# Performance work log

Measured on AMD Instinct MI355X. Metric: run time of the kernel, lower is better.

Reference implementation:

```python
import jax, jax.numpy as jnp
import numpy as np
from jax import lax

EPS = 1e-5  # BatchNorm1d default eps

def setup_inputs() -> dict:
    key = jax.random.key(0)
    ks = jax.random.split(key, 8)
    B, IN, H, T = 1024, 128, 256, 256
    return {
        "inputs": jax.random.normal(ks[0], (B, IN), jnp.float32),
        "hidden": jnp.zeros((B, H), jnp.float32),
        "W_ih": jax.random.normal(ks[1], (3 * H, IN), jnp.float32) * 0.05,
        "b_ih": jax.random.normal(ks[2], (3 * H,), jnp.float32) * 0.05,
        "W_hh": jax.random.normal(ks[3], (3 * H, H), jnp.float32) * 0.05,
        "b_hh": jax.random.normal(ks[4], (3 * H,), jnp.float32) * 0.05,
        "W_lin": jax.random.normal(ks[5], (IN, H), jnp.float32) * 0.05,
        "b_lin": jax.random.normal(ks[6], (IN,), jnp.float32) * 0.05,
        "n_frames": 256,
    }

def reference(inputs, hidden, W_ih, b_ih, W_hh, b_hh, W_lin, b_lin, n_frames):
    def step(carry, _):
        x, h = carry
        gi = x @ W_ih.T + b_ih          # [B, 3H]
        gh = h @ W_hh.T + b_hh          # [B, 3H]
        i_r, i_z, i_n = jnp.split(gi, 3, axis=-1)
        h_r, h_z, h_n = jnp.split(gh, 3, axis=-1)
        r = jax.nn.sigmoid(i_r + h_r)
        z = jax.nn.sigmoid(i_z + h_z)
        n = jnp.tanh(i_n + r * h_n)
        h_new = (1.0 - z) * n + z * h   # GRUCell update
        y = h_new @ W_lin.T + b_lin     # fed back as next input
        return (y, h_new), y

    _, ys = lax.scan(step, (inputs, hidden), None, length=n_frames)  # [T, B, out]
    # BatchNorm1d(affine=False), training mode: biased batch stats per timestep
    mean = jnp.mean(ys, axis=1, keepdims=True)
    var = jnp.var(ys, axis=1, keepdims=True)
    return (ys - mean) / jnp.sqrt(var + EPS)
```

## Files before the change

kernel.cpp:

```cpp
#include <hip/hip_runtime.h>


typedef _Float16 half8 __attribute__((ext_vector_type(8)));
typedef float floatx4 __attribute__((ext_vector_type(4)));
typedef unsigned uintx4 __attribute__((ext_vector_type(4)));

#define EPS_BN 1e-5f

#define WS_WC 0
#define WS_W0 524288
#define WS_WL 1114112
#define WS_B0 1179648
#define WS_BC 1183744
#define WS_ST 1187840

static __device__ __forceinline__ unsigned short f2h(float f) {
    union { _Float16 h; unsigned short u; } v;
    v.h = (_Float16)f;
    return v.u;
}
static __device__ __forceinline__ half8 as_h8(uint4 v) {
    union { uint4 u; half8 h; } x; x.u = v; return x.h;
}
static __device__ __forceinline__ half8 ld_agpr(const uint4* p) {
    uintx4 v = *(const uintx4*)p;
    asm volatile("; wpin" : "+a"(v));
    union { uintx4 u; half8 h; } x; x.u = v; return x.h;
}
static __device__ __forceinline__ float sigm(float x) {
    return __builtin_amdgcn_rcpf(1.0f + __builtin_amdgcn_exp2f(-1.442695041f * x));
}
static __device__ __forceinline__ float tanh_fast(float x) {
    return 1.0f - 2.0f * __builtin_amdgcn_rcpf(1.0f + __builtin_amdgcn_exp2f(2.885390082f * x));
}
static __device__ __forceinline__ void bar_lgkm() {
    asm volatile("s_waitcnt lgkmcnt(0)\n\ts_barrier" ::: "memory");
}
#define MFMA16(A, B, C) __builtin_amdgcn_mfma_f32_16x16x32_f16((A), (B), (C), 0, 0, 0)

__global__ void pack_w0_kernel(const float* __restrict__ W_ih, const float* __restrict__ W_hh,
                               const float* __restrict__ W_lin, const float* __restrict__ b_ih,
                               const float* __restrict__ b_hh,
                               uint4* __restrict__ w0, uint4* __restrict__ wl,
                               float4* __restrict__ bias0)
{
    int i = blockIdx.x * 256 + threadIdx.x;
    if (i < 36864) {
        int lane = i & 63, tile = i >> 6;
        int w = tile / 36, rem = tile - w * 36;
        int g = rem / 12, kt = rem - g * 12;
        int n = g * 256 + (w << 4) + (lane & 15);
        int k0 = (kt << 5) + ((lane >> 4) << 3);
        const float* p = (k0 < 128) ? (W_ih + n * 128 + k0)
                                    : (W_hh + n * 256 + (k0 - 128));
        unsigned short h[8];
        #pragma unroll
        for (int j = 0; j < 8; ++j) h[j] = f2h(p[j]);
        uint4 v;
        v.x = (unsigned)h[0] | ((unsigned)h[1] << 16);
        v.y = (unsigned)h[2] | ((unsigned)h[3] << 16);
        v.z = (unsigned)h[4] | ((unsigned)h[5] << 16);
        v.w = (unsigned)h[6] | ((unsigned)h[7] << 16);
        w0[i] = v;
    } else if (i < 40960) {
        int i2 = i - 36864;
        int lane = i2 & 63, tile = i2 >> 6;
        int n = (tile >> 3) * 16 + (lane & 15);
        int k0 = ((tile & 7) << 5) + ((lane >> 4) << 3);
        const float* p = W_lin + n * 256 + k0;
        unsigned short h[8];
        #pragma unroll
        for (int j = 0; j < 8; ++j) h[j] = f2h(p[j]);
        uint4 v;
        v.x = (unsigned)h[0] | ((unsigned)h[1] << 16);
        v.y = (unsigned)h[2] | ((unsigned)h[3] << 16);
        v.z = (unsigned)h[4] | ((unsigned)h[5] << 16);
        v.w = (unsigned)h[6] | ((unsigned)h[7] << 16);
        wl[i2] = v;
    } else if (i < 41216) {
        int cb = i - 40960;
        bias0[cb] = make_float4(b_ih[cb] + b_hh[cb],
                                b_ih[256 + cb] + b_hh[256 + cb],
                                b_ih[512 + cb], b_hh[512 + cb]);
    }
}

__global__ void pack_wc_kernel(const float* __restrict__ W_ih, const float* __restrict__ W_hh,
                               const float* __restrict__ W_lin, const float* __restrict__ b_ih,
                               const float* __restrict__ b_hh, const float* __restrict__ b_lin,
                               uint4* __restrict__ wc, float4* __restrict__ bc)
{
    int i = blockIdx.x * 256 + threadIdx.x;
    if (i < 32768) {
        int lane = i & 63, tile = i >> 6;
        int w = tile >> 5, r = tile & 31;
        int g = r >> 3, kt = r & 7;
        int c = (w << 4) + (lane & 15);
        int k0 = (kt << 5) + ((lane >> 4) << 3);
        float s[8];
        if (g == 3) {
            #pragma unroll
            for (int j = 0; j < 8; ++j) s[j] = W_hh[(512 + c) * 256 + k0 + j];
        } else {
            int row = g * 256 + c;
            const float* wi = W_ih + row * 128;
            #pragma unroll
            for (int j = 0; j < 8; ++j) s[j] = 0.0f;
            for (int ii = 0; ii < 128; ++ii) {
                float wv = wi[ii];
                const float* wrow = W_lin + ii * 256 + k0;
                #pragma unroll
                for (int j = 0; j < 8; ++j) s[j] += wv * wrow[j];
            }
            if (g < 2) {
                #pragma unroll
                for (int j = 0; j < 8; ++j) s[j] += W_hh[row * 256 + k0 + j];
            }
        }
        unsigned short h[8];
        #pragma unroll
        for (int j = 0; j < 8; ++j) h[j] = f2h(s[j]);
        uint4 v;
        v.x = (unsigned)h[0] | ((unsigned)h[1] << 16);
        v.y = (unsigned)h[2] | ((unsigned)h[3] << 16);
        v.z = (unsigned)h[4] | ((unsigned)h[5] << 16);
        v.w = (unsigned)h[6] | ((unsigned)h[7] << 16);
        wc[i] = v;
    } else if (i < 33024) {
        int c = i - 32768;
        float d0 = 0.f, d1 = 0.f, d2 = 0.f;
        for (int ii = 0; ii < 128; ++ii) {
            float bl = b_lin[ii];
            d0 += bl * W_ih[c * 128 + ii];
            d1 += bl * W_ih[(256 + c) * 128 + ii];
            d2 += bl * W_ih[(512 + c) * 128 + ii];
        }
        bc[c] = make_float4(b_ih[c] + b_hh[c] + d0,
                            b_ih[256 + c] + b_hh[256 + c] + d1,
                            b_ih[512 + c] + d2,
                            b_hh[512 + c]);
    }
}

__global__ __launch_bounds__(512, 2) void gru_kernel(
    const float* __restrict__ inputs,
    const float* __restrict__ hidden,
    const uint4* __restrict__ wc,
    const uint4* __restrict__ w0,
    const float4* __restrict__ bias0,
    const float4* __restrict__ bcp,
    float* __restrict__ out)
{
    __shared__ uint4 lds[9472];

    const int tid  = threadIdx.x;
    const int lane = tid & 63;
    const int w    = tid >> 6;
    const int quad = lane >> 4;
    const int nc   = lane & 15;
    const int r0   = blockIdx.x << 4;
    const int c0   = (w << 4) + nc;
    const int c1   = 128 + c0;
    const float4 bc0 = bcp[c0];
    const float4 bc1 = bcp[c1];
    const uint4* wcw0 = wc + (size_t)w * 2048;
    const uint4* wcw1 = wc + (size_t)(w + 8) * 2048;

    half8 wr0[8], wz0[8], wr1[8], wz1[8];
    #pragma unroll
    for (int kt = 0; kt < 8; ++kt) {
        wr0[kt] = ld_agpr(&wcw0[kt * 64 + lane]);
        wz0[kt] = ld_agpr(&wcw0[(8 + kt) * 64 + lane]);
        wr1[kt] = ld_agpr(&wcw1[kt * 64 + lane]);
        wz1[kt] = ld_agpr(&wcw1[(8 + kt) * 64 + lane]);
    }

    const int wbase = 1280 + (w << 10);
    #pragma unroll
    for (int i = 0; i < 4; ++i) {
        lds[wbase + (i << 6) + lane]             = wcw0[(16 + i) * 64 + lane];
        lds[wbase + ((4 + i) << 6) + lane]       = wcw0[(24 + i) * 64 + lane];
        lds[wbase + 512 + (i << 6) + lane]       = wcw1[(16 + i) * 64 + lane];
        lds[wbase + 512 + ((4 + i) << 6) + lane] = wcw1[(24 + i) * 64 + lane];
    }

    float hreg[8];
    #pragma unroll
    for (int d = 0; d < 4; ++d) {
        hreg[d]     = hidden[(r0 + (quad << 2) + d) * 256 + c0];
        hreg[4 + d] = hidden[(r0 + (quad << 2) + d) * 256 + c1];
    }

    unsigned short* lds_u16 = (unsigned short*)lds;
    const int kp  = ((w & 1) << 4) + nc;
    const int lf  = ((kp >> 3) << 4) + (quad << 2);
    const int hfb0 = (((w >> 1) * 64 + lf) << 3) + (kp & 7);
    const int hfb1 = (((4 + (w >> 1)) * 64 + lf) << 3) + (kp & 7);

    for (int idx = tid; idx < 2048; idx += 512) {
        int ktl = idx >> 8;
        int rem = idx & 255;
        int lfr = rem >> 2, jg = rem & 3;
        int m = lfr & 15;
        int hc = ktl * 32 + (lfr >> 4) * 8 + jg * 2;
        const float* p = hidden + (r0 + m) * 256 + hc;
        unsigned pk = (unsigned)f2h(p[0]) | ((unsigned)f2h(p[1]) << 16);
        ((unsigned*)lds)[(ktl * 64 + lfr) * 4 + jg] = pk;
    }
    for (int idx = tid; idx < 1024; idx += 512) {
        int kt = idx >> 8, lfr = (idx >> 2) & 63, jg = idx & 3;
        int m = lfr & 15;
        int k0 = (kt << 5) + ((lfr >> 4) << 3) + (jg << 1);
        const float* p = inputs + (r0 + m) * 128 + k0;
        unsigned pk = (unsigned)f2h(p[0]) | ((unsigned)f2h(p[1]) << 16);
        ((unsigned*)lds)[(1024 + (kt << 6) + lfr) * 4 + jg] = pk;
    }
    __syncthreads();

    unsigned short* Hout = (unsigned short*)out;

    {
        #pragma unroll
        for (int g2 = 0; g2 < 2; ++g2) {
            const uint4* ww = w0 + (size_t)(g2 ? (w + 8) : w) * 2304;
            floatx4 ar = {0.f,0.f,0.f,0.f}, az = {0.f,0.f,0.f,0.f};
            floatx4 ain = {0.f,0.f,0.f,0.f}, ahn = {0.f,0.f,0.f,0.f};
            #pragma unroll
            for (int kt = 0; kt < 12; ++kt) {
                half8 A = as_h8(kt < 4 ? lds[1024 + (kt << 6) + lane]
                                       : lds[((kt - 4) << 6) + lane]);
                ar = MFMA16(A, as_h8(ww[kt * 64 + lane]), ar);
                az = MFMA16(A, as_h8(ww[(12 + kt) * 64 + lane]), az);
                if (kt < 4)
                    ain = MFMA16(A, as_h8(ww[(24 + kt) * 64 + lane]), ain);
                else
                    ahn = MFMA16(A, as_h8(ww[(24 + kt) * 64 + lane]), ahn);
            }
            const int cc = g2 ? c1 : c0;
            const int hfb = g2 ? hfb1 : hfb0;
            float4 b0 = bias0[cc];
            #pragma unroll
            for (int d = 0; d < 4; ++d) {
                float rr = sigm(ar[d] + b0.x);
                float zz = sigm(az[d] + b0.y);
                float nn = tanh_fast(ain[d] + b0.z + rr * (ahn[d] + b0.w));
                float hnew = (1.0f - zz) * nn + zz * hreg[(g2 << 2) + d];
                hreg[(g2 << 2) + d] = hnew;
                unsigned short hu = f2h(hnew);
                lds_u16[4096 + hfb + (d << 3)] = hu;
                Hout[((size_t)(r0 + (quad << 2) + d) << 8) + cc] = hu;
            }
        }
        bar_lgkm();
    }

    for (int t = 1; t < 256; ++t) {
        const int rb   = (t & 1) << 9;
        const int wb16 = (((t + 1) & 1) << 9) << 3;

        const uint4* s0p = wcw0 + lane;
        const uint4* s1p = wcw1 + lane;
        asm("" : "+v"(s0p), "+v"(s1p));

        uint4 si0[4], sh0[4], si1[4], sh1[4];
        si0[0] = s0p[20 * 64]; sh0[0] = s0p[28 * 64];
        si1[0] = s1p[20 * 64]; sh1[0] = s1p[28 * 64];

        floatx4 ar0 = {0.f,0.f,0.f,0.f}, az0 = {0.f,0.f,0.f,0.f};
        floatx4 ai0 = {0.f,0.f,0.f,0.f}, ah0 = {0.f,0.f,0.f,0.f};
        floatx4 ar1 = {0.f,0.f,0.f,0.f}, az1 = {0.f,0.f,0.f,0.f};
        floatx4 ai1 = {0.f,0.f,0.f,0.f}, ah1 = {0.f,0.f,0.f,0.f};

        #pragma unroll
        for (int kt = 0; kt < 8; ++kt) {
            half8 A = as_h8(lds[rb + (kt << 6) + lane]);
            if (kt == 1) {
                si0[1] = s0p[21 * 64]; sh0[1] = s0p[29 * 64];
                si1[1] = s1p[21 * 64]; sh1[1] = s1p[29 * 64];
            }
            if (kt == 2) {
                si0[2] = s0p[22 * 64]; sh0[2] = s0p[30 * 64];
                si1[2] = s1p[22 * 64]; sh1[2] = s1p[30 * 64];
            }
            if (kt == 3) {
                si0[3] = s0p[23 * 64]; sh0[3] = s0p[31 * 64];
                si1[3] = s1p[23 * 64]; sh1[3] = s1p[31 * 64];
            }
            ar0 = MFMA16(A, wr0[kt], ar0);
            ar1 = MFMA16(A, wr1[kt], ar1);
            az0 = MFMA16(A, wz0[kt], az0);
            az1 = MFMA16(A, wz1[kt], az1);
            half8 Bi0 = (kt < 4) ? as_h8(lds[wbase + (kt << 6) + lane])
                                 : as_h8(si0[kt - 4]);
            half8 Bi1 = (kt < 4) ? as_h8(lds[wbase + 512 + (kt << 6) + lane])
                                 : as_h8(si1[kt - 4]);
            ai0 = MFMA16(A, Bi0, ai0);
            ai1 = MFMA16(A, Bi1, ai1);
            half8 Bh0 = (kt < 4) ? as_h8(lds[wbase + ((4 + kt) << 6) + lane])
                                 : as_h8(sh0[kt - 4]);
            half8 Bh1 = (kt < 4) ? as_h8(lds[wbase + 512 + ((4 + kt) << 6) + lane])
                                 : as_h8(sh1[kt - 4]);
            ah0 = MFMA16(A, Bh0, ah0);
            ah1 = MFMA16(A, Bh1, ah1);
        }

        const size_t obase = (size_t)t * 1024 + r0 + (quad << 2);
        #pragma unroll
        for (int d = 0; d < 4; ++d) {
            float rr = sigm(ar0[d] + bc0.x);
            float zz = sigm(az0[d] + bc0.y);
            float nn = tanh_fast(ai0[d] + bc0.z + rr * (ah0[d] + bc0.w));
            float hnew = (1.0f - zz) * nn + zz * hreg[d];
            hreg[d] = hnew;
            unsigned short hu = f2h(hnew);
            lds_u16[wb16 + hfb0 + (d << 3)] = hu;
            Hout[((obase + d) << 8) + c0] = hu;
        }
        #pragma unroll
        for (int d = 0; d < 4; ++d) {
            float rr = sigm(ar1[d] + bc1.x);
            float zz = sigm(az1[d] + bc1.y);
            float nn = tanh_fast(ai1[d] + bc1.z + rr * (ah1[d] + bc1.w));
            float hnew = (1.0f - zz) * nn + zz * hreg[4 + d];
            hreg[4 + d] = hnew;
            unsigned short hu = f2h(hnew);
            lds_u16[wb16 + hfb1 + (d << 3)] = hu;
            Hout[((obase + d) << 8) + c1] = hu;
        }
        bar_lgkm();
    }
}

__global__ __launch_bounds__(256) void ygemm_kernel(
    const uint4* __restrict__ wl, const float* __restrict__ b_lin,
    float* __restrict__ out, float* __restrict__ stats)
{
    __shared__ unsigned short sh[16 * 264];
    const int tid = threadIdx.x;
    const int t = blockIdx.x >> 6;
    const int r0 = (blockIdx.x & 63) << 4;

    {
        int row = tid >> 4, seg = tid & 15;
        const uint4* src = (const uint4*)((const unsigned short*)out
                         + (((size_t)t << 10) + r0 + row) * 256) + (seg << 1);
        uint4 a = src[0], b = src[1];
        uint4* dst = (uint4*)(sh + row * 264 + (seg << 4));
        dst[0] = a; dst[1] = b;
    }
    __syncthreads();

    const int lane = tid & 63, w = tid >> 6;
    const int quad = lane >> 4, nc = lane & 15;
    const int m = lane & 15, khi = lane >> 4;

    half8 B0[8], B1[8];
    #pragma unroll
    for (int kt = 0; kt < 8; ++kt) {
        B0[kt] = as_h8(wl[(((w << 1) + 0) * 8 + kt) * 64 + lane]);
        B1[kt] = as_h8(wl[(((w << 1) + 1) * 8 + kt) * 64 + lane]);
    }
    floatx4 a0 = {0.f,0.f,0.f,0.f}, a1 = {0.f,0.f,0.f,0.f};
    #pragma unroll
    for (int kt = 0; kt < 8; ++kt) {
        half8 A = *(const half8*)(sh + m * 264 + (kt << 5) + (khi << 3));
        a0 = MFMA16(A, B0[kt], a0);
        a1 = MFMA16(A, B1[kt], a1);
    }
    #pragma unroll
    for (int g = 0; g < 2; ++g) {
        floatx4 acc = g ? a1 : a0;
        int i = (((w << 1) + g) << 4) + nc;
        float bl = b_lin[i];
        float s1 = 0.f, s2 = 0.f;
        float* orow = out + (((size_t)t << 10) + r0 + (quad << 2)) * 128 + i;
        #pragma unroll
        for (int d = 0; d < 4; ++d) {
            float y = acc[d] + bl;
            orow[(size_t)d << 7] = y;
            s1 += y; s2 += y * y;
        }
        s1 += __shfl_xor(s1, 16); s1 += __shfl_xor(s1, 32);
        s2 += __shfl_xor(s2, 16); s2 += __shfl_xor(s2, 32);
        if (lane < 16) {
            int si = ((t << 7) + (((w << 1) + g) << 4) + lane) << 1;
            atomicAdd(&stats[si], s1);
            atomicAdd(&stats[si + 1], s2);
        }
    }
}

__global__ void norm_kernel(float* __restrict__ out, const float* __restrict__ stats)
{
    __shared__ float smean[128], sscale[128];
    int t = blockIdx.x >> 2, q = blockIdx.x & 3;
    int tid = threadIdx.x;
    if (tid < 128) {
        int si = ((t << 7) + tid) << 1;
        float mean = stats[si] * (1.0f / 1024.0f);
        float var = stats[si + 1] * (1.0f / 1024.0f) - mean * mean;
        smean[tid] = mean;
        sscale[tid] = rsqrtf(var + EPS_BN);
    }
    __syncthreads();
    float4* p = (float4*)(out + ((size_t)t << 17) + ((size_t)q << 15));
    for (int i = tid; i < 8192; i += 256) {
        int cc = (i & 31) << 2;
        float4 v = p[i];
        v.x = (v.x - smean[cc])     * sscale[cc];
        v.y = (v.y - smean[cc + 1]) * sscale[cc + 1];
        v.z = (v.z - smean[cc + 2]) * sscale[cc + 2];
        v.w = (v.w - smean[cc + 3]) * sscale[cc + 3];
        p[i] = v;
    }
}

extern "C" void kernel_launch(void* const* d_in, const int* in_sizes, int n_in,
                              void* d_out, int out_size, void* d_ws, size_t ws_size,
                              hipStream_t stream) {
    (void)in_sizes; (void)n_in; (void)out_size; (void)ws_size;
    const float* inputs = (const float*)d_in[0];
    const float* hidden = (const float*)d_in[1];
    const float* W_ih   = (const float*)d_in[2];
    const float* b_ih   = (const float*)d_in[3];
    const float* W_hh   = (const float*)d_in[4];
    const float* b_hh   = (const float*)d_in[5];
    const float* W_lin  = (const float*)d_in[6];
    const float* b_lin  = (const float*)d_in[7];

    char* ws = (char*)d_ws;
    uint4*  wcp   = (uint4*)(ws + WS_WC);
    uint4*  w0p   = (uint4*)(ws + WS_W0);
    uint4*  wlp   = (uint4*)(ws + WS_WL);
    float4* bias0 = (float4*)(ws + WS_B0);
    float4* bcp   = (float4*)(ws + WS_BC);
    float*  stats = (float*)(ws + WS_ST);

    hipMemsetAsync(stats, 0, 262144, stream);
    pack_w0_kernel<<<161, 256, 0, stream>>>(W_ih, W_hh, W_lin, b_ih, b_hh, w0p, wlp, bias0);
    pack_wc_kernel<<<129, 256, 0, stream>>>(W_ih, W_hh, W_lin, b_ih, b_hh, b_lin, wcp, bcp);
    gru_kernel<<<64, 512, 0, stream>>>(inputs, hidden, wcp, w0p, bias0, bcp, (float*)d_out);
    ygemm_kernel<<<16384, 256, 0, stream>>>(wlp, b_lin, (float*)d_out, stats);
    norm_kernel<<<1024, 256, 0, stream>>>((float*)d_out, stats);
}
```

Before: 1.047 ms.

## Fuse output GEMM with BatchNorm per timestep and merge packing kernels

The separate y-GEMM, atomic statistics accumulation, memset and normalization kernels are replaced by one kernel per timestep. It computes y from the fp16 hidden states, reduces mean and variance in shared memory, and writes normalized outputs from y held as fp16 in AGPRs. The two weight-packing kernels are merged into one launch. This removes a global round trip of y, the global atomics and several launches. In exchange, y is rounded to fp16 before normalization and register pressure is high, which limits occupancy.

```diff
diff --git a/kernel.cpp b/kernel.cpp
--- a/kernel.cpp
+++ b/kernel.cpp
@@ -12,13 +12,19 @@
 #define WS_WL 1114112
 #define WS_B0 1179648
 #define WS_BC 1183744
-#define WS_ST 1187840
 
 static __device__ __forceinline__ unsigned short f2h(float f) {
     union { _Float16 h; unsigned short u; } v;
     v.h = (_Float16)f;
     return v.u;
 }
+static __device__ __forceinline__ unsigned pack2h(float a, float b) {
+    return (unsigned)f2h(a) | ((unsigned)f2h(b) << 16);
+}
+static __device__ __forceinline__ float2 up2(unsigned u) {
+    union { unsigned v; _Float16 h[2]; } x; x.v = u;
+    return make_float2((float)x.h[0], (float)x.h[1]);
+}
 static __device__ __forceinline__ half8 as_h8(uint4 v) {
     union { uint4 u; half8 h; } x; x.u = v; return x.h;
 }
@@ -38,59 +44,56 @@
 }
 #define MFMA16(A, B, C) __builtin_amdgcn_mfma_f32_16x16x32_f16((A), (B), (C), 0, 0, 0)
 
-__global__ void pack_w0_kernel(const float* __restrict__ W_ih, const float* __restrict__ W_hh,
-                               const float* __restrict__ W_lin, const float* __restrict__ b_ih,
-                               const float* __restrict__ b_hh,
-                               uint4* __restrict__ w0, uint4* __restrict__ wl,
-                               float4* __restrict__ bias0)
+__global__ void pack_all_kernel(const float* __restrict__ W_ih, const float* __restrict__ W_hh,
+                                const float* __restrict__ W_lin, const float* __restrict__ b_ih,
+                                const float* __restrict__ b_hh, const float* __restrict__ b_lin,
+                                uint4* __restrict__ w0, uint4* __restrict__ wl,
+                                float4* __restrict__ bias0,
+                                uint4* __restrict__ wc, float4* __restrict__ bc)
 {
-    int i = blockIdx.x * 256 + threadIdx.x;
-    if (i < 36864) {
-        int lane = i & 63, tile = i >> 6;
-        int w = tile / 36, rem = tile - w * 36;
-        int g = rem / 12, kt = rem - g * 12;
-        int n = g * 256 + (w << 4) + (lane & 15);
-        int k0 = (kt << 5) + ((lane >> 4) << 3);
-        const float* p = (k0 < 128) ? (W_ih + n * 128 + k0)
-                                    : (W_hh + n * 256 + (k0 - 128));
-        unsigned short h[8];
-        #pragma unroll
-        for (int j = 0; j < 8; ++j) h[j] = f2h(p[j]);
-        uint4 v;
-        v.x = (unsigned)h[0] | ((unsigned)h[1] << 16);
-        v.y = (unsigned)h[2] | ((unsigned)h[3] << 16);
-        v.z = (unsigned)h[4] | ((unsigned)h[5] << 16);
-        v.w = (unsigned)h[6] | ((unsigned)h[7] << 16);
-        w0[i] = v;
-    } else if (i < 40960) {
-        int i2 = i - 36864;
-        int lane = i2 & 63, tile = i2 >> 6;
-        int n = (tile >> 3) * 16 + (lane & 15);
-        int k0 = ((tile & 7) << 5) + ((lane >> 4) << 3);
-        const float* p = W_lin + n * 256 + k0;
-        unsigned short h[8];
-        #pragma unroll
-        for (int j = 0; j < 8; ++j) h[j] = f2h(p[j]);
-        uint4 v;
-        v.x = (unsigned)h[0] | ((unsigned)h[1] << 16);
-        v.y = (unsigned)h[2] | ((unsigned)h[3] << 16);
-        v.z = (unsigned)h[4] | ((unsigned)h[5] << 16);
-        v.w = (unsigned)h[6] | ((unsigned)h[7] << 16);
-        wl[i2] = v;
-    } else if (i < 41216) {
-        int cb = i - 40960;
-        bias0[cb] = make_float4(b_ih[cb] + b_hh[cb],
-                                b_ih[256 + cb] + b_hh[256 + cb],
-                                b_ih[512 + cb], b_hh[512 + cb]);
-    }
-}
-
-__global__ void pack_wc_kernel(const float* __restrict__ W_ih, const float* __restrict__ W_hh,
-                               const float* __restrict__ W_lin, const float* __restrict__ b_ih,
-                               const float* __restrict__ b_hh, const float* __restrict__ b_lin,
-                               uint4* __restrict__ wc, float4* __restrict__ bc)
-{
-    int i = blockIdx.x * 256 + threadIdx.x;
+    if (blockIdx.x < 161) {
+        int i = blockIdx.x * 256 + threadIdx.x;
+        if (i < 36864) {
+            int lane = i & 63, tile = i >> 6;
+            int w = tile / 36, rem = tile - w * 36;
+            int g = rem / 12, kt = rem - g * 12;
+            int n = g * 256 + (w << 4) + (lane & 15);
+            int k0 = (kt << 5) + ((lane >> 4) << 3);
+            const float* p = (k0 < 128) ? (W_ih + n * 128 + k0)
+                                        : (W_hh + n * 256 + (k0 - 128));
+            unsigned short h[8];
+            #pragma unroll
+            for (int j = 0; j < 8; ++j) h[j] = f2h(p[j]);
+            uint4 v;
+            v.x = (unsigned)h[0] | ((unsigned)h[1] << 16);
+            v.y = (unsigned)h[2] | ((unsigned)h[3] << 16);
+            v.z = (unsigned)h[4] | ((unsigned)h[5] << 16);
+            v.w = (unsigned)h[6] | ((unsigned)h[7] << 16);
+            w0[i] = v;
+        } else if (i < 40960) {
+            int i2 = i - 36864;
+            int lane = i2 & 63, tile = i2 >> 6;
+            int n = (tile >> 3) * 16 + (lane & 15);
+            int k0 = ((tile & 7) << 5) + ((lane >> 4) << 3);
+            const float* p = W_lin + n * 256 + k0;
+            unsigned short h[8];
+            #pragma unroll
+            for (int j = 0; j < 8; ++j) h[j] = f2h(p[j]);
+            uint4 v;
+            v.x = (unsigned)h[0] | ((unsigned)h[1] << 16);
+            v.y = (unsigned)h[2] | ((unsigned)h[3] << 16);
+            v.z = (unsigned)h[4] | ((unsigned)h[5] << 16);
+            v.w = (unsigned)h[6] | ((unsigned)h[7] << 16);
+            wl[i2] = v;
+        } else if (i < 41216) {
+            int cb = i - 40960;
+            bias0[cb] = make_float4(b_ih[cb] + b_hh[cb],
+                                    b_ih[256 + cb] + b_hh[256 + cb],
+                                    b_ih[512 + cb], b_hh[512 + cb]);
+        }
+        return;
+    }
+    int i = (blockIdx.x - 161) * 256 + threadIdx.x;
     if (i < 32768) {
         int lane = i & 63, tile = i >> 6;
         int w = tile >> 5, r = tile & 31;
@@ -331,87 +334,121 @@
     }
 }
 
-__global__ __launch_bounds__(256) void ygemm_kernel(
+__global__ __launch_bounds__(512, 2) void yfused_kernel(
     const uint4* __restrict__ wl, const float* __restrict__ b_lin,
-    float* __restrict__ out, float* __restrict__ stats)
+    float* __restrict__ out)
 {
-    __shared__ unsigned short sh[16 * 264];
-    const int tid = threadIdx.x;
-    const int t = blockIdx.x >> 6;
-    const int r0 = (blockIdx.x & 63) << 4;
-
-    {
-        int row = tid >> 4, seg = tid & 15;
-        const uint4* src = (const uint4*)((const unsigned short*)out
-                         + (((size_t)t << 10) + r0 + row) * 256) + (seg << 1);
-        uint4 a = src[0], b = src[1];
-        uint4* dst = (uint4*)(sh + row * 264 + (seg << 4));
-        dst[0] = a; dst[1] = b;
-    }
+    __shared__ uint4 bfr[4096];
+    __shared__ float sred[8][256];
+    __shared__ float snorm[256];
+
+    const int tid  = threadIdx.x;
+    const int lane = tid & 63;
+    const int w    = tid >> 6;
+    const int quad = lane >> 4;
+    const int nc   = lane & 15;
+    const int t    = blockIdx.x;
+
+    const unsigned short* H = (const unsigned short*)out + (size_t)t * 262144;
+    float* Y = out + (size_t)t * 131072;
+
+    #pragma unroll
+    for (int i = 0; i < 8; ++i)
+        bfr[(i << 9) + tid] = wl[(i << 9) + tid];
+
+    float blv[8];
+    #pragma unroll
+    for (int c = 0; c < 8; ++c) blv[c] = b_lin[(c << 4) + nc];
+
     __syncthreads();
 
-    const int lane = tid & 63, w = tid >> 6;
-    const int quad = lane >> 4, nc = lane & 15;
-    const int m = lane & 15, khi = lane >> 4;
-
-    half8 B0[8], B1[8];
-    #pragma unroll
-    for (int kt = 0; kt < 8; ++kt) {
-        B0[kt] = as_h8(wl[(((w << 1) + 0) * 8 + kt) * 64 + lane]);
-        B1[kt] = as_h8(wl[(((w << 1) + 1) * 8 + kt) * 64 + lane]);
-    }
-    floatx4 a0 = {0.f,0.f,0.f,0.f}, a1 = {0.f,0.f,0.f,0.f};
-    #pragma unroll
-    for (int kt = 0; kt < 8; ++kt) {
-        half8 A = *(const half8*)(sh + m * 264 + (kt << 5) + (khi << 3));
-        a0 = MFMA16(A, B0[kt], a0);
-        a1 = MFMA16(A, B1[kt], a1);
-    }
-    #pragma unroll
-    for (int g = 0; g < 2; ++g) {
-        floatx4 acc = g ? a1 : a0;
-        int i = (((w << 1) + g) << 4) + nc;
-        float bl = b_lin[i];
-        float s1 = 0.f, s2 = 0.f;
-        float* orow = out + (((size_t)t << 10) + r0 + (quad << 2)) * 128 + i;
-        #pragma unroll
-        for (int d = 0; d < 4; ++d) {
-            float y = acc[d] + bl;
-            orow[(size_t)d << 7] = y;
-            s1 += y; s2 += y * y;
-        }
-        s1 += __shfl_xor(s1, 16); s1 += __shfl_xor(s1, 32);
-        s2 += __shfl_xor(s2, 16); s2 += __shfl_xor(s2, 32);
-        if (lane < 16) {
-            int si = ((t << 7) + (((w << 1) + g) << 4) + lane) << 1;
-            atomicAdd(&stats[si], s1);
-            atomicAdd(&stats[si + 1], s2);
-        }
-    }
-}
-
-__global__ void norm_kernel(float* __restrict__ out, const float* __restrict__ stats)
-{
-    __shared__ float smean[128], sscale[128];
-    int t = blockIdx.x >> 2, q = blockIdx.x & 3;
-    int tid = threadIdx.x;
+    const int rw0 = w << 7;
+    float s1[8], s2[8];
+    #pragma unroll
+    for (int c = 0; c < 8; ++c) { s1[c] = 0.f; s2[c] = 0.f; }
+    uintx4 ypk[32];
+
+    #pragma unroll
+    for (int s = 0; s < 8; ++s) {
+        const unsigned short* hrow = H + (size_t)(rw0 + (s << 4) + nc) * 256 + (quad << 3);
+        uint4 A[8];
+        #pragma unroll
+        for (int kt = 0; kt < 8; ++kt)
+            A[kt] = *(const uint4*)(hrow + (kt << 5));
+        unsigned te0 = 0, te1 = 0;
+        #pragma unroll
+        for (int c = 0; c < 8; ++c) {
+            floatx4 acc = {0.f, 0.f, 0.f, 0.f};
+            #pragma unroll
+            for (int kt = 0; kt < 8; ++kt)
+                acc = MFMA16(as_h8(A[kt]), as_h8(bfr[(((c << 3) + kt) << 6) + lane]), acc);
+            float y0 = acc[0] + blv[c], y1 = acc[1] + blv[c];
+            float y2 = acc[2] + blv[c], y3 = acc[3] + blv[c];
+            s1[c] += (y0 + y1) + (y2 + y3);
+            s2[c] += (y0 * y0 + y1 * y1) + (y2 * y2 + y3 * y3);
+            unsigned q0 = pack2h(y0, y1), q1 = pack2h(y2, y3);
+            if ((c & 1) == 0) { te0 = q0; te1 = q1; }
+            else {
+                uintx4 v; v[0] = te0; v[1] = te1; v[2] = q0; v[3] = q1;
+                asm volatile("; ypin" : "+a"(v));
+                ypk[(s << 2) + (c >> 1)] = v;
+            }
+        }
+    }
+
+    #pragma unroll
+    for (int c = 0; c < 8; ++c) {
+        s1[c] += __shfl_xor(s1[c], 16); s1[c] += __shfl_xor(s1[c], 32);
+        s2[c] += __shfl_xor(s2[c], 16); s2[c] += __shfl_xor(s2[c], 32);
+    }
+    if (lane < 16) {
+        #pragma unroll
+        for (int c = 0; c < 8; ++c) {
+            sred[w][(c << 4) + lane]       = s1[c];
+            sred[w][128 + (c << 4) + lane] = s2[c];
+        }
+    }
+    __syncthreads();
     if (tid < 128) {
-        int si = ((t << 7) + tid) << 1;
-        float mean = stats[si] * (1.0f / 1024.0f);
-        float var = stats[si + 1] * (1.0f / 1024.0f) - mean * mean;
-        smean[tid] = mean;
-        sscale[tid] = rsqrtf(var + EPS_BN);
+        float a1 = 0.f, a2 = 0.f;
+        #pragma unroll
+        for (int w2 = 0; w2 < 8; ++w2) {
+            a1 += sred[w2][tid];
+            a2 += sred[w2][128 + tid];
+        }
+        float mean = a1 * (1.0f / 1024.0f);
+        float var  = a2 * (1.0f / 1024.0f) - mean * mean;
+        snorm[tid]       = mean;
+        snorm[128 + tid] = rsqrtf(var + EPS_BN);
     }
     __syncthreads();
-    float4* p = (float4*)(out + ((size_t)t << 17) + ((size_t)q << 15));
-    for (int i = tid; i < 8192; i += 256) {
-        int cc = (i & 31) << 2;
-        float4 v = p[i];
-        v.x = (v.x - smean[cc])     * sscale[cc];
-        v.y = (v.y - smean[cc + 1]) * sscale[cc + 1];
-        v.z = (v.z - smean[cc + 2]) * sscale[cc + 2];
-        v.w = (v.w - smean[cc + 3]) * sscale[cc + 3];
-        p[i] = v;
+
+    float mn[8], scl[8];
+    #pragma unroll
+    for (int c = 0; c < 8; ++c) {
+        mn[c]  = snorm[(c << 4) + nc];
+        scl[c] = snorm[128 + (c << 4) + nc];
+    }
+
+    #pragma unroll
+    for (int s = 0; s < 8; ++s) {
+        float* yrow = Y + (size_t)(rw0 + (s << 4) + (quad << 2)) * 128 + nc;
+        #pragma unroll
+        for (int cp = 0; cp < 4; ++cp) {
+            uintx4 v = ypk[(s << 2) + cp];
+            const int c0 = cp << 1, c1 = c0 + 1;
+            float2 a01 = up2(v[0]), a23 = up2(v[1]);
+            float2 b01 = up2(v[2]), b23 = up2(v[3]);
+            const int o0 = cp << 5, o1 = o0 + 16;
+            yrow[0 * 128 + o0] = (a01.x - mn[c0]) * scl[c0];
+            yrow[1 * 128 + o0] = (a01.y - mn[c0]) * scl[c0];
+            yrow[2 * 128 + o0] = (a23.x - mn[c0]) * scl[c0];
+            yrow[3 * 128 + o0] = (a23.y - mn[c0]) * scl[c0];
+            yrow[0 * 128 + o1] = (b01.x - mn[c1]) * scl[c1];
+            yrow[1 * 128 + o1] = (b01.y - mn[c1]) * scl[c1];
+            yrow[2 * 128 + o1] = (b23.x - mn[c1]) * scl[c1];
+            yrow[3 * 128 + o1] = (b23.y - mn[c1]) * scl[c1];
+        }
     }
 }
 
@@ -434,12 +471,9 @@
     uint4*  wlp   = (uint4*)(ws + WS_WL);
     float4* bias0 = (float4*)(ws + WS_B0);
     float4* bcp   = (float4*)(ws + WS_BC);
-    float*  stats = (float*)(ws + WS_ST);
-
-    hipMemsetAsync(stats, 0, 262144, stream);
-    pack_w0_kernel<<<161, 256, 0, stream>>>(W_ih, W_hh, W_lin, b_ih, b_hh, w0p, wlp, bias0);
-    pack_wc_kernel<<<129, 256, 0, stream>>>(W_ih, W_hh, W_lin, b_ih, b_hh, b_lin, wcp, bcp);
+
+    pack_all_kernel<<<290, 256, 0, stream>>>(W_ih, W_hh, W_lin, b_ih, b_hh, b_lin,
+                                             w0p, wlp, bias0, wcp, bcp);
     gru_kernel<<<64, 512, 0, stream>>>(inputs, hidden, wcp, w0p, bias0, bcp, (float*)d_out);
-    ygemm_kernel<<<16384, 256, 0, stream>>>(wlp, b_lin, (float*)d_out, stats);
-    norm_kernel<<<1024, 256, 0, stream>>>((float*)d_out, stats);
-}
+    yfused_kernel<<<256, 512, 0, stream>>>(wlp, b_lin, (float*)d_out);
+}
```

New measurement: 1.001 ms. -4.4%, faster.
